# Optimization experiments

Measured on AMD Instinct MI355X. Metric: run time of the kernel, lower is better.

The kernel has to match this reference:

```python
import jax, jax.numpy as jnp
import numpy as np

L = 32        # label_num = len(label2idx)
SOS = 0       # label2idx['[SOS]']
END = 1       # label2idx['[END]']
NEG = -10000.0
B, T = 512, 1024


def setup_inputs() -> dict:
    key = jax.random.key(0)
    k1, k2, k3 = jax.random.split(key, 3)
    emission = jax.random.normal(k1, (B, T, L), dtype=jnp.float32)
    label_ids = jax.random.randint(k2, (B, T), 0, L)
    transitions = jax.random.normal(k3, (L, L), dtype=jnp.float32)
    # CrfLayer.__init__: forbid transitions into [SOS] and out of [END]
    transitions = transitions.at[SOS, :].set(NEG).at[:, END].set(NEG)
    return {"emission": emission, "label_ids": label_ids, "transitions": transitions}


def reference(emission, label_ids, transitions):
    b, t, l = emission.shape
    # ---- _forward_alg: log-partition via sequential logsumexp recurrence ----
    alpha0 = jnp.full((b, l), NEG, dtype=emission.dtype).at[:, SOS].set(0.0)
    feats_t = jnp.transpose(emission, (1, 0, 2))  # [T, B, L]

    def step(alpha, feat):
        # aa[b, j, i] = alpha[b, i] + feat[b, j] + transitions[j, i]
        aa = alpha[:, None, :] + feat[:, :, None] + transitions[None, :, :]
        return jax.nn.logsumexp(aa, axis=2), None

    alpha, _ = jax.lax.scan(step, alpha0, feats_t)
    forward_score = jax.nn.logsumexp(alpha + transitions[END][None, :], axis=1)  # [B]

    # ---- _score_sentence: score of the gold path ----
    tags = jnp.concatenate(
        [jnp.full((b, 1), SOS, dtype=label_ids.dtype), label_ids], axis=1)  # [B, T+1]
    trans_score = transitions[tags[:, 1:], tags[:, :-1]].sum(axis=1)          # [B]
    emit_score = jnp.take_along_axis(
        emission, tags[:, 1:, None].astype(jnp.int32), axis=2)[..., 0].sum(axis=1)  # [B]
    gold_score = trans_score + emit_score + transitions[END, tags[:, -1]]

    # loss = sum(forward_score - gold_score)
    return jnp.sum(forward_score - gold_score)
```

## Files before the change

kernel.cpp:

```cpp
#include <hip/hip_runtime.h>


typedef float  f32x16 __attribute__((ext_vector_type(16)));
typedef short  s16x8  __attribute__((ext_vector_type(8)));
typedef float  f32x2  __attribute__((ext_vector_type(2)));
typedef float  f32x4  __attribute__((ext_vector_type(4)));

#define TT 1024
#define LL 32
#define BB 512
#define NC 8
#define CL 128
#define MS 33

union Frag { s16x8 v; unsigned u[4]; };

__device__ __forceinline__ unsigned pack_bf16(float lo, float hi) {
    return __builtin_amdgcn_perm(__float_as_uint(hi), __float_as_uint(lo), 0x07060302u);
}

__global__ __launch_bounds__(NC * 64, 4) void crf_fused_kernel(
    const float* __restrict__ emission,
    const int*   __restrict__ label_ids,
    const float* __restrict__ transitions,
    float*       __restrict__ out)
{
    __shared__ __align__(16) float shM[NC][32 * MS];
    __shared__ __align__(16) float shF[NC][32];
    __shared__ float shQ[2][64];
    __shared__ float tgArr[NC];
    __shared__ int   capArr[NC];

    const int tid  = threadIdx.x;
    const int w    = tid >> 6;
    const int lane = tid & 63;
    const int j    = lane & 31;
    const int h    = lane >> 5;
    const int b    = blockIdx.x;
    const int t0   = w * CL;

    const int*   labB = label_ids + b * TT + t0;
    const float* emB  = emission + ((size_t)b * TT + t0) * LL + j;

    {
        float g = 0.0f;
#pragma unroll
        for (int u = 0; u < 2; ++u) {
            int tt = t0 + 64 * u + lane;
            int l1 = labB[64 * u + lane];
            int l0 = (tt == 0) ? 0 : label_ids[b * TT + tt - 1];
            g += transitions[(l1 << 5) + l0];
            g += emission[((size_t)b * TT + tt) * LL + l1];
            if (tt == TT - 1) g += transitions[32 + l1];
        }
#pragma unroll
        for (int m = 32; m >= 1; m >>= 1) g += __shfl_xor(g, m, 64);
        if (lane == 0) tgArr[w] = g;
    }

    const float* trow = transitions + j * 32;
    Frag Ea0, Ea1;
#pragma unroll
    for (int p = 0; p < 4; ++p) {
        int c0 = ((2 * p) & 3)     + 8 * ((2 * p) >> 2)     + 4 * h;
        int c1 = ((2 * p + 1) & 3) + 8 * ((2 * p + 1) >> 2) + 4 * h;
        Ea0.u[p] = pack_bf16(__expf(trow[c0]),      __expf(trow[c1]));
        Ea1.u[p] = pack_bf16(__expf(trow[16 + c0]), __expf(trow[16 + c1]));
    }

    Frag B0, B1;
#pragma unroll
    for (int i = 0; i < 8; ++i) {
        int row = (i & 3) + 8 * (i >> 2) + 4 * h;
        B0.v[i] = (short)((row == j)      ? 0x3F80 : 0);
        B1.v[i] = (short)((row + 16 == j) ? 0x3F80 : 0);
    }

    f32x16 acc;

    float ring[8];
#pragma unroll
    for (int s = 0; s < 8; ++s) ring[s] = emB[s * LL];

    shF[w][j] = __expf(ring[0]);
    const f32x4* fp = (const f32x4*)(&shF[w][0]);
    f32x4 fA = fp[h], fB = fp[2 + h], fC = fp[4 + h], fD = fp[6 + h];

    float sc = 1.0f;
    int   Cap = 0, elast = 0;

    auto step = [&](int k, int s, bool refill, bool last) {
#pragma unroll
        for (int i = 0; i < 16; ++i) acc[i] = 0.0f;
        asm volatile("s_nop 1\n\t"
                     "v_mfma_f32_32x32x16_bf16 %0, %1, %2, %0\n\t"
                     "v_mfma_f32_32x32x16_bf16 %0, %3, %4, %0\n\t"
                     "s_nop 7\n\t"
                     "s_nop 3"
                     : "+v"(acc)
                     : "v"(Ea0.v), "v"(B0.v), "v"(Ea1.v), "v"(B1.v));

        if ((s & 3) == 3) {
            int pb = __builtin_amdgcn_readlane(__float_as_int(acc[2]), 0);
            int e  = ((pb >> 23) & 0xff) - 127;
            sc = __int_as_float((127 - e) << 23);
            Cap += e;
            elast = e;
        }

        {
            float fn = __expf(ring[(k + 1) & 7]);
            if (((s + 1) & 3) == 0) fn *= sc;
            shF[w][j] = fn;
        }
        f32x4 nA = fp[h], nB = fp[2 + h], nC = fp[4 + h], nD = fp[6 + h];

        if (refill) ring[k] = emB[(s + 8) * LL];

        f32x2 t0v[4], t1v[4];
        {
            f32x2 fv, av;
            fv[0] = fA[0]; fv[1] = fA[1]; av[0] = acc[0];  av[1] = acc[1];  t0v[0] = fv * av;
            fv[0] = fA[2]; fv[1] = fA[3]; av[0] = acc[2];  av[1] = acc[3];  t0v[1] = fv * av;
            fv[0] = fB[0]; fv[1] = fB[1]; av[0] = acc[4];  av[1] = acc[5];  t0v[2] = fv * av;
            fv[0] = fB[2]; fv[1] = fB[3]; av[0] = acc[6];  av[1] = acc[7];  t0v[3] = fv * av;
            fv[0] = fC[0]; fv[1] = fC[1]; av[0] = acc[8];  av[1] = acc[9];  t1v[0] = fv * av;
            fv[0] = fC[2]; fv[1] = fC[3]; av[0] = acc[10]; av[1] = acc[11]; t1v[1] = fv * av;
            fv[0] = fD[0]; fv[1] = fD[1]; av[0] = acc[12]; av[1] = acc[13]; t1v[2] = fv * av;
            fv[0] = fD[2]; fv[1] = fD[3]; av[0] = acc[14]; av[1] = acc[15]; t1v[3] = fv * av;
        }
#pragma unroll
        for (int q = 0; q < 4; ++q) {
            B0.u[q] = pack_bf16(t0v[q][0], t0v[q][1]);
            B1.u[q] = pack_bf16(t1v[q][0], t1v[q][1]);
        }

        if (last) {
#pragma unroll
            for (int r = 0; r < 16; ++r) {
                int row = (r & 3) + 8 * (r >> 2) + 4 * h;
                float val = (r < 8) ? t0v[r >> 1][r & 1] : t1v[(r >> 1) - 4][r & 1];
                shM[w][row * MS + j] = val;
            }
        }

        fA = nA; fB = nB; fC = nC; fD = nD;
    };

    for (int s0 = 0; s0 < CL - 8; s0 += 8) {
#pragma unroll
        for (int k = 0; k < 8; ++k) step(k, s0 + k, true, false);
    }
#pragma unroll
    for (int k = 0; k < 8; ++k) step(k, CL - 8 + k, false, k == 7);

    Cap -= elast;
    if (lane == 0) capArr[w] = Cap;

    __syncthreads();

    if (w == 0) {
        const float Eend = __expf(transitions[32 + j]);
        float q = (j == 0) ? 1.0f : 0.0f;
        int   Cq = 0;
        float gold = 0.0f;

#pragma unroll
        for (int c = 0; c < NC; ++c) {
            shQ[c & 1][lane] = q;
            asm volatile("s_waitcnt lgkmcnt(0)" ::: "memory");
            __builtin_amdgcn_wave_barrier();
            const float* Mrow = &shM[c][j * MS];
            const float* qv   = &shQ[c & 1][h * 32];
            float a0 = 0.f, a1 = 0.f, a2 = 0.f, a3 = 0.f;
#pragma unroll
            for (int i = 0; i < 32; i += 4) {
                a0 = fmaf(Mrow[i],     qv[i],     a0);
                a1 = fmaf(Mrow[i + 1], qv[i + 1], a1);
                a2 = fmaf(Mrow[i + 2], qv[i + 2], a2);
                a3 = fmaf(Mrow[i + 3], qv[i + 3], a3);
            }
            float qn = (a0 + a1) + (a2 + a3);
            int pb = __builtin_amdgcn_readlane(__float_as_int(qn), 2);
            int e  = ((pb >> 23) & 0xff) - 127;
            qn *= __int_as_float((127 - e) << 23);
            Cq += e + capArr[c];
            gold += tgArr[c];
            q = qn;
        }

        float v = q * Eend;
#pragma unroll
        for (int m = 16; m >= 1; m >>= 1) v += __shfl_xor(v, m, 32);
        float fwd = __logf(v) + (float)Cq * 0.69314718055994531f;

        if (lane == 0) atomicAdd(out, fwd - gold);
    }
}

extern "C" void kernel_launch(void* const* d_in, const int* in_sizes, int n_in,
                              void* d_out, int out_size, void* d_ws, size_t ws_size,
                              hipStream_t stream)
{
    const float* emission    = (const float*)d_in[0];
    const int*   label_ids   = (const int*)d_in[1];
    const float* transitions = (const float*)d_in[2];
    float* out = (float*)d_out;

    (void)hipMemsetAsync(out, 0, sizeof(float), stream);
    crf_fused_kernel<<<BB, NC * 64, 0, stream>>>(emission, label_ids, transitions, out);
}
```

Before: 142.3 us.

## Interleave two independent chunk recurrences per wave to hide MFMA latency

Each wave now runs two independent 128-step chunk recurrences interleaved, with 4 waves per block instead of 8. Before, each step stalled on explicit s_nop padding after the dependent MFMA pair. Alternating two chains lets one chunk's MFMA latency overlap the other's exp/pack/LDS work, and the inline asm is replaced by compiler builtins. The cost is more registers per wave (launch bounds drop to 2 blocks) and fewer waves per block, which may cut occupancy and memory-latency hiding.

```diff
diff --git a/kernel.cpp b/kernel.cpp
--- a/kernel.cpp
+++ b/kernel.cpp
@@ -9,7 +9,8 @@
 #define TT 1024
 #define LL 32
 #define BB 512
-#define NC 8
+#define NW 4
+#define CH 8
 #define CL 128
 #define MS 33
 
@@ -19,17 +20,17 @@
     return __builtin_amdgcn_perm(__float_as_uint(hi), __float_as_uint(lo), 0x07060302u);
 }
 
-__global__ __launch_bounds__(NC * 64, 4) void crf_fused_kernel(
+__global__ __launch_bounds__(NW * 64, 2) void crf_fused_kernel(
     const float* __restrict__ emission,
     const int*   __restrict__ label_ids,
     const float* __restrict__ transitions,
     float*       __restrict__ out)
 {
-    __shared__ __align__(16) float shM[NC][32 * MS];
-    __shared__ __align__(16) float shF[NC][32];
+    __shared__ __align__(16) float shM[CH][32 * MS];
+    __shared__ __align__(16) float shF[CH][32];
     __shared__ float shQ[2][64];
-    __shared__ float tgArr[NC];
-    __shared__ int   capArr[NC];
+    __shared__ float tgArr[NW];
+    __shared__ int   capArr[CH];
 
     const int tid  = threadIdx.x;
     const int w    = tid >> 6;
@@ -37,15 +38,13 @@
     const int j    = lane & 31;
     const int h    = lane >> 5;
     const int b    = blockIdx.x;
-    const int t0   = w * CL;
-
-    const int*   labB = label_ids + b * TT + t0;
-    const float* emB  = emission + ((size_t)b * TT + t0) * LL + j;
+    const int t0   = w * (2 * CL);
 
     {
+        const int* labB = label_ids + b * TT + t0;
         float g = 0.0f;
 #pragma unroll
-        for (int u = 0; u < 2; ++u) {
+        for (int u = 0; u < 4; ++u) {
             int tt = t0 + 64 * u + lane;
             int l1 = labB[64 * u + lane];
             int l0 = (tt == 0) ? 0 : label_ids[b * TT + tt - 1];
@@ -68,37 +67,41 @@
         Ea1.u[p] = pack_bf16(__expf(trow[16 + c0]), __expf(trow[16 + c1]));
     }
 
-    Frag B0, B1;
+    Frag B0a, B1a, B0b, B1b;
 #pragma unroll
     for (int i = 0; i < 8; ++i) {
         int row = (i & 3) + 8 * (i >> 2) + 4 * h;
-        B0.v[i] = (short)((row == j)      ? 0x3F80 : 0);
-        B1.v[i] = (short)((row + 16 == j) ? 0x3F80 : 0);
-    }
-
-    f32x16 acc;
-
-    float ring[8];
-#pragma unroll
-    for (int s = 0; s < 8; ++s) ring[s] = emB[s * LL];
-
-    shF[w][j] = __expf(ring[0]);
-    const f32x4* fp = (const f32x4*)(&shF[w][0]);
-    f32x4 fA = fp[h], fB = fp[2 + h], fC = fp[4 + h], fD = fp[6 + h];
-
-    float sc = 1.0f;
-    int   Cap = 0, elast = 0;
-
-    auto step = [&](int k, int s, bool refill, bool last) {
-#pragma unroll
-        for (int i = 0; i < 16; ++i) acc[i] = 0.0f;
-        asm volatile("s_nop 1\n\t"
-                     "v_mfma_f32_32x32x16_bf16 %0, %1, %2, %0\n\t"
-                     "v_mfma_f32_32x32x16_bf16 %0, %3, %4, %0\n\t"
-                     "s_nop 7\n\t"
-                     "s_nop 3"
-                     : "+v"(acc)
-                     : "v"(Ea0.v), "v"(B0.v), "v"(Ea1.v), "v"(B1.v));
+        short lo = (short)((row == j)      ? 0x3F80 : 0);
+        short hi = (short)((row + 16 == j) ? 0x3F80 : 0);
+        B0a.v[i] = lo;  B1a.v[i] = hi;
+        B0b.v[i] = lo;  B1b.v[i] = hi;
+    }
+
+    f32x16 zc, accA, accB;
+#pragma unroll
+    for (int i = 0; i < 16; ++i) zc[i] = 0.0f;
+
+    const float* emA  = emission + ((size_t)b * TT + t0) * LL + j;
+    const float* emBp = emA + (size_t)CL * LL;
+
+    float ringA[8], ringB[8];
+#pragma unroll
+    for (int s = 0; s < 8; ++s) { ringA[s] = emA[s * LL]; ringB[s] = emBp[s * LL]; }
+
+    shF[2 * w][j]     = __expf(ringA[0]);
+    shF[2 * w + 1][j] = __expf(ringB[0]);
+
+    float scA = 1.0f, scB = 1.0f;
+    int   CapA = 0, elA = 0, CapB = 0, elB = 0;
+
+    auto step = [&](Frag& B0, Frag& B1, f32x16& acc, float (&ring)[8],
+                    float& sc, int& Cap, int& elast, const float* em,
+                    float* shFc, int cidx, int k, int s, bool refill, bool last) {
+        const f32x4* fp = (const f32x4*)shFc;
+        f32x4 fA = fp[h], fB = fp[2 + h], fC = fp[4 + h], fD = fp[6 + h];
+
+        acc = __builtin_amdgcn_mfma_f32_32x32x16_bf16(Ea0.v, B0.v, zc, 0, 0, 0);
+        acc = __builtin_amdgcn_mfma_f32_32x32x16_bf16(Ea1.v, B1.v, acc, 0, 0, 0);
 
         if ((s & 3) == 3) {
             int pb = __builtin_amdgcn_readlane(__float_as_int(acc[2]), 0);
@@ -111,11 +114,10 @@
         {
             float fn = __expf(ring[(k + 1) & 7]);
             if (((s + 1) & 3) == 0) fn *= sc;
-            shF[w][j] = fn;
-        }
-        f32x4 nA = fp[h], nB = fp[2 + h], nC = fp[4 + h], nD = fp[6 + h];
-
-        if (refill) ring[k] = emB[(s + 8) * LL];
+            shFc[j] = fn;
+        }
+
+        if (refill) ring[k] = em[(s + 8) * LL];
 
         f32x2 t0v[4], t1v[4];
         {
@@ -140,22 +142,31 @@
             for (int r = 0; r < 16; ++r) {
                 int row = (r & 3) + 8 * (r >> 2) + 4 * h;
                 float val = (r < 8) ? t0v[r >> 1][r & 1] : t1v[(r >> 1) - 4][r & 1];
-                shM[w][row * MS + j] = val;
+                shM[cidx][row * MS + j] = val;
             }
         }
-
-        fA = nA; fB = nB; fC = nC; fD = nD;
     };
 
     for (int s0 = 0; s0 < CL - 8; s0 += 8) {
 #pragma unroll
-        for (int k = 0; k < 8; ++k) step(k, s0 + k, true, false);
-    }
-#pragma unroll
-    for (int k = 0; k < 8; ++k) step(k, CL - 8 + k, false, k == 7);
-
-    Cap -= elast;
-    if (lane == 0) capArr[w] = Cap;
+        for (int k = 0; k < 8; ++k) {
+            step(B0a, B1a, accA, ringA, scA, CapA, elA, emA,
+                 &shF[2 * w][0],     2 * w,     k, s0 + k, true, false);
+            step(B0b, B1b, accB, ringB, scB, CapB, elB, emBp,
+                 &shF[2 * w + 1][0], 2 * w + 1, k, s0 + k, true, false);
+        }
+    }
+#pragma unroll
+    for (int k = 0; k < 8; ++k) {
+        step(B0a, B1a, accA, ringA, scA, CapA, elA, emA,
+             &shF[2 * w][0],     2 * w,     k, CL - 8 + k, false, k == 7);
+        step(B0b, B1b, accB, ringB, scB, CapB, elB, emBp,
+             &shF[2 * w + 1][0], 2 * w + 1, k, CL - 8 + k, false, k == 7);
+    }
+
+    CapA -= elA;
+    CapB -= elB;
+    if (lane == 0) { capArr[2 * w] = CapA; capArr[2 * w + 1] = CapB; }
 
     __syncthreads();
 
@@ -163,10 +174,9 @@
         const float Eend = __expf(transitions[32 + j]);
         float q = (j == 0) ? 1.0f : 0.0f;
         int   Cq = 0;
-        float gold = 0.0f;
-
-#pragma unroll
-        for (int c = 0; c < NC; ++c) {
+
+#pragma unroll
+        for (int c = 0; c < CH; ++c) {
             shQ[c & 1][lane] = q;
             asm volatile("s_waitcnt lgkmcnt(0)" ::: "memory");
             __builtin_amdgcn_wave_barrier();
@@ -185,9 +195,12 @@
             int e  = ((pb >> 23) & 0xff) - 127;
             qn *= __int_as_float((127 - e) << 23);
             Cq += e + capArr[c];
-            gold += tgArr[c];
             q = qn;
         }
+
+        float gold = 0.0f;
+#pragma unroll
+        for (int c = 0; c < NW; ++c) gold += tgArr[c];
 
         float v = q * Eend;
 #pragma unroll
@@ -208,5 +221,5 @@
     float* out = (float*)d_out;
 
     (void)hipMemsetAsync(out, 0, sizeof(float), stream);
-    crf_fused_kernel<<<BB, NC * 64, 0, stream>>>(emission, label_ids, transitions, out);
+    crf_fused_kernel<<<BB, NW * 64, 0, stream>>>(emission, label_ids, transitions, out);
 }
```

Measured after the change: 138.6 us. 2.6% less time.
